# Kernel tuning notes

Measured on AMD Instinct MI355X. Metric: run time of the kernel, lower is better.

Reference implementation:

```python
import jax, jax.numpy as jnp
import numpy as np

B, S, D = 4, 4096, 64
D_MODEL = 64


def setup_inputs() -> dict:
    key = jax.random.key(0)
    kq, kk, kv, km = jax.random.split(key, 4)
    q = jax.random.normal(kq, (B, S, D), dtype=jnp.float32)
    k = jax.random.normal(kk, (B, S, D), dtype=jnp.float32)
    v = jax.random.normal(kv, (B, S, D), dtype=jnp.float32)
    mask = jax.random.uniform(km, (B, S, S), dtype=jnp.float32)
    return {"q": q, "k": k, "v": v, "mask": mask}


def reference(q, k, v, mask):
    dk = jnp.sqrt(jnp.asarray(D_MODEL, dtype=q.dtype))
    # [B,S,S] scores; multiplicative (non-additive) mask applied pre-softmax
    scaled_qk = jnp.einsum('bqd,bkd->bqk', q, k) / dk
    scaled_qk = scaled_qk * mask
    attn = jax.nn.softmax(scaled_qk, axis=-1)
    return jnp.einsum('bqk,bkd->bqd', attn, v)
```

## Files before the change

### kernel.cpp

```cpp
#include <hip/hip_runtime.h>
#include <hip/hip_bf16.h>

#define S_LEN 4096
#define DH 64
#define NBATCH 4

typedef __attribute__((ext_vector_type(8))) short bf16x8;
typedef __attribute__((ext_vector_type(4))) short bf16x4;
typedef __attribute__((ext_vector_type(4))) float f32x4;

static __device__ __forceinline__ short f2bf(float x) {
  __hip_bfloat16 h = __float2bfloat16(x);
  return *reinterpret_cast<short*>(&h);
}

#define MFMA(a, b, c) __builtin_amdgcn_mfma_f32_16x16x32_bf16((a), (b), (c), 0, 0, 0)

__global__ __launch_bounds__(256) void cvt_q_kernel(const float* __restrict__ q,
                                                    short* __restrict__ qb) {
  int i = (blockIdx.x * 256 + threadIdx.x) * 4;
  f32x4 x = *(const f32x4*)(q + i);
  bf16x4 o;
#pragma unroll
  for (int j = 0; j < 4; ++j) o[j] = f2bf(x[j]);
  *(bf16x4*)(qb + i) = o;
}

__global__ __launch_bounds__(256) void cvt_frag_kernel(const float* __restrict__ k,
                                                       const float* __restrict__ v,
                                                       short* __restrict__ kfrag,
                                                       short* __restrict__ vfrag) {
  __shared__ short kt[32][80];
  __shared__ short vt[32][80];
  const int t = threadIdx.x;
  const int b = blockIdx.x >> 7;
  const int i = blockIdx.x & 127;
  const size_t src0 = ((size_t)b * S_LEN + i * 32) * DH;
  {
    const int row = t >> 3, c0 = (t & 7) * 8;
    const f32x4 xk0 = *(const f32x4*)(k + src0 + row * DH + c0);
    const f32x4 xk1 = *(const f32x4*)(k + src0 + row * DH + c0 + 4);
    const f32x4 xv0 = *(const f32x4*)(v + src0 + row * DH + c0);
    const f32x4 xv1 = *(const f32x4*)(v + src0 + row * DH + c0 + 4);
#pragma unroll
    for (int j = 0; j < 4; ++j) {
      kt[row][c0 + j] = f2bf(xk0[j]);  kt[row][c0 + 4 + j] = f2bf(xk1[j]);
      vt[row][c0 + j] = f2bf(xv0[j]);  vt[row][c0 + 4 + j] = f2bf(xv1[j]);
    }
  }
  __syncthreads();
  const int c = t >> 6, l = t & 63;
  const size_t dst = (((size_t)(b * 128 + i) * 4 + c) * 64 + l) * 8;
  {
    const int kr = ((c >> 1) * 16) + (l & 15);
    const int d0 = ((c & 1) * 32) + (l >> 4) * 8;
    *(bf16x8*)(kfrag + dst) = *(const bf16x8*)&kt[kr][d0];
  }
  {
    bf16x8 f;
    const int col = c * 16 + (l & 15);
    const int r0 = (l >> 4) * 8;
#pragma unroll
    for (int j = 0; j < 8; ++j) f[j] = vt[r0 + j][col];
    *(bf16x8*)(vfrag + dst) = f;
  }
}

__global__ __launch_bounds__(512, 2) void fa_kernel(
    const short* __restrict__ qb, const short* __restrict__ kfrag,
    const short* __restrict__ vfrag, const float* __restrict__ mask,
    float* __restrict__ out) {
  __shared__ __align__(16) short kst[2][2][4][512];
  __shared__ __align__(16) short vst[2][2][4][512];
  __shared__ __align__(16) float mst[2][4096];
  __shared__ __align__(16) short lds_p[8][16][40];
  __shared__ float lds_O[8][16][64];
  __shared__ float lds_l[8][16];

  const int tid = threadIdx.x;
  const int w = tid >> 6;
  const int wq = w >> 1;
  const int wk = w & 1;
  const int lane = tid & 63;
  const int quad = lane >> 4;
  const int n16 = lane & 15;
  const int loff = lane * 8;

  const int vb = ((blockIdx.x & 7) << 5) | (blockIdx.x >> 3);
  const int b = vb >> 6;
  const int q0 = (vb & 63) << 6;

  const int qr = q0 + wq * 16 + n16;
  const short* qrow = qb + (size_t)(b * S_LEN + qr) * DH;
  const bf16x8 aQ0 = *(const bf16x8*)(qrow + quad * 8);
  const bf16x8 aQ1 = *(const bf16x8*)(qrow + 32 + quad * 8);

  f32x4 O0 = {0.f, 0.f, 0.f, 0.f}, O1 = O0, O2 = O0, O3 = O0;
  float lacc = 0.f;

  const int ksp = w >> 2, kfr = w & 3;
  const short* kbase =
      kfrag + (size_t)(b * 128 + ksp) * 2048 + kfr * 512 + loff;
  const short* vbase =
      vfrag + (size_t)(b * 128 + ksp) * 2048 + kfr * 512 + loff;
  const int srow0 = w * 8 + (lane >> 4);
  const int srow1 = srow0 + 4;
  const int sg = lane & 15;
  const float* msrc0 =
      mask + ((size_t)b * S_LEN + q0 + srow0) * S_LEN + sg * 4;
  const float* msrc1 =
      mask + ((size_t)b * S_LEN + q0 + srow1) * S_LEN + sg * 4;
  const int wslot0 = srow0 * 64 + (sg ^ (srow0 & 7)) * 4;
  const int wslot1 = srow1 * 64 + (sg ^ (srow1 & 7)) * 4;
  const int mr = wq * 16 + n16;
  const int rslot0 = mr * 64 + (((wk * 8 + quad) ^ (mr & 7)) * 4);
  const int rslot1 = mr * 64 + (((wk * 8 + 4 + quad) ^ (mr & 7)) * 4);

#define STEP(CUR, SS)                                                      \
  {                                                                        \
    const int sn_ = ((SS) + 1) & 63; \
    const bf16x8 kR = *(const bf16x8*)(kbase + (size_t)sn_ * 4096);        \
    const bf16x8 vR = *(const bf16x8*)(vbase + (size_t)sn_ * 4096);        \
    const f32x4 mR0 = *(const f32x4*)(msrc0 + sn_ * 64);                   \
    const f32x4 mR1 = *(const f32x4*)(msrc1 + sn_ * 64);                   \
    const f32x4 z = {0.f, 0.f, 0.f, 0.f};                                  \
    f32x4 s0 = MFMA(*(const bf16x8*)&kst[CUR][wk][0][loff], aQ0, z);       \
    s0 = MFMA(*(const bf16x8*)&kst[CUR][wk][1][loff], aQ1, s0);            \
    f32x4 s1 = MFMA(*(const bf16x8*)&kst[CUR][wk][2][loff], aQ0, z);       \
    s1 = MFMA(*(const bf16x8*)&kst[CUR][wk][3][loff], aQ1, s1);            \
    const f32x4 M0 = *(const f32x4*)&mst[CUR][rslot0];                     \
    const f32x4 M1 = *(const f32x4*)&mst[CUR][rslot1];                     \
    float p0_[4], p1_[4];                                                  \
    _Pragma("unroll") for (int r = 0; r < 4; ++r) {                        \
      p0_[r] = __expf(s0[r] * 0.125f * M0[r]);                             \
      p1_[r] = __expf(s1[r] * 0.125f * M1[r]);                             \
      lacc += p0_[r] + p1_[r];                                             \
    }                                                                      \
    bf16x4 w0_, w1_;                                                       \
    _Pragma("unroll") for (int r = 0; r < 4; ++r) {                        \
      w0_[r] = f2bf(p0_[r]); w1_[r] = f2bf(p1_[r]);                        \
    }                                                                      \
    *(bf16x4*)&lds_p[w][n16][quad * 4] = w0_;                              \
    *(bf16x4*)&lds_p[w][n16][16 + quad * 4] = w1_;                         \
    const bf16x8 aP = *(const bf16x8*)&lds_p[w][n16][quad * 8];            \
    O0 = MFMA(aP, *(const bf16x8*)&vst[CUR][wk][0][loff], O0);             \
    O1 = MFMA(aP, *(const bf16x8*)&vst[CUR][wk][1][loff], O1);             \
    O2 = MFMA(aP, *(const bf16x8*)&vst[CUR][wk][2][loff], O2);             \
    O3 = MFMA(aP, *(const bf16x8*)&vst[CUR][wk][3][loff], O3);             \
    *(bf16x8*)&kst[(CUR) ^ 1][ksp][kfr][loff] = kR;                        \
    *(bf16x8*)&vst[(CUR) ^ 1][ksp][kfr][loff] = vR;                        \
    *(f32x4*)&mst[(CUR) ^ 1][wslot0] = mR0;                                \
    *(f32x4*)&mst[(CUR) ^ 1][wslot1] = mR1;                                \
    __syncthreads();                                                       \
  }

  {
    const bf16x8 kR = *(const bf16x8*)(kbase);
    const bf16x8 vR = *(const bf16x8*)(vbase);
    const f32x4 mR0 = *(const f32x4*)(msrc0);
    const f32x4 mR1 = *(const f32x4*)(msrc1);
    *(bf16x8*)&kst[0][ksp][kfr][loff] = kR;
    *(bf16x8*)&vst[0][ksp][kfr][loff] = vR;
    *(f32x4*)&mst[0][wslot0] = mR0;
    *(f32x4*)&mst[0][wslot1] = mR1;
    __syncthreads();
  }

#pragma unroll 1
  for (int it = 0; it < 32; ++it) {
    STEP(0, 2 * it);
    STEP(1, 2 * it + 1);
  }
#undef STEP

  lacc += __shfl_xor(lacc, 16);
  lacc += __shfl_xor(lacc, 32);

#pragma unroll
  for (int r = 0; r < 4; ++r) {
    const int row = quad * 4 + r;
    lds_O[w][row][n16]      = O0[r];
    lds_O[w][row][16 + n16] = O1[r];
    lds_O[w][row][32 + n16] = O2[r];
    lds_O[w][row][48 + n16] = O3[r];
  }
  if (lane < 16) lds_l[w][lane] = lacc;
  __syncthreads();

  const int g = tid >> 7;
  const int r = (tid >> 3) & 15;
  const int c8 = (tid & 7) << 3;
  const int w0 = g * 2, w1 = g * 2 + 1;
  const float inv = 1.0f / (lds_l[w0][r] + lds_l[w1][r]);
  float* op = out + (size_t)(b * S_LEN + q0 + g * 16 + r) * DH + c8;
  f32x4 acc0, acc1;
#pragma unroll
  for (int j = 0; j < 4; ++j) {
    acc0[j] = (lds_O[w0][r][c8 + j]     + lds_O[w1][r][c8 + j])     * inv;
    acc1[j] = (lds_O[w0][r][c8 + 4 + j] + lds_O[w1][r][c8 + 4 + j]) * inv;
  }
  *(f32x4*)(op) = acc0;
  *(f32x4*)(op + 4) = acc1;
}

extern "C" void kernel_launch(void* const* d_in, const int* in_sizes, int n_in,
                              void* d_out, int out_size, void* d_ws, size_t ws_size,
                              hipStream_t stream) {
  const float* q = (const float*)d_in[0];
  const float* k = (const float*)d_in[1];
  const float* v = (const float*)d_in[2];
  const float* mask = (const float*)d_in[3];
  float* out = (float*)d_out;

  short* qb = (short*)d_ws;
  short* kfrag = qb + (size_t)NBATCH * S_LEN * DH;
  short* vfrag = kfrag + (size_t)NBATCH * S_LEN * DH;

  cvt_q_kernel<<<(NBATCH * S_LEN * DH) / 1024, 256, 0, stream>>>(q, qb);
  cvt_frag_kernel<<<NBATCH * 128, 256, 0, stream>>>(k, v, kfrag, vfrag);
  fa_kernel<<<NBATCH * 64, 512, 0, stream>>>(qb, kfrag, vfrag, mask, out);
}
```

Baseline: 393.4 us.

## Stage K/V/mask tiles via direct global-to-LDS loads with triple buffering

Replaces the register-staged double buffer with a three-deep LDS ring filled by global_load_lds, so K, V and mask tiles skip VGPRs and arrive two steps ahead. The XOR swizzle for the mask moves into the global source address, and a single waitcnt plus barrier per step replaces the per-step syncthreads. The epilogue buffers reuse the staging memory to keep LDS use in check. The cost is a larger LDS footprint, which may reduce blocks per CU, and a correctness risk from hand-written waitcnt accounting.

```diff
diff --git a/kernel.cpp b/kernel.cpp
--- a/kernel.cpp
+++ b/kernel.cpp
@@ -12,6 +12,12 @@
 static __device__ __forceinline__ short f2bf(float x) {
   __hip_bfloat16 h = __float2bfloat16(x);
   return *reinterpret_cast<short*>(&h);
+}
+
+static __device__ __forceinline__ void gl_lds16(const void* g, void* l) {
+  __builtin_amdgcn_global_load_lds(
+      (const __attribute__((address_space(1))) void*)g,
+      (__attribute__((address_space(3))) void*)l, 16, 0, 0);
 }
 
 #define MFMA(a, b, c) __builtin_amdgcn_mfma_f32_16x16x32_bf16((a), (b), (c), 0, 0, 0)
@@ -70,12 +76,8 @@
     const short* __restrict__ qb, const short* __restrict__ kfrag,
     const short* __restrict__ vfrag, const float* __restrict__ mask,
     float* __restrict__ out) {
-  __shared__ __align__(16) short kst[2][2][4][512];
-  __shared__ __align__(16) short vst[2][2][4][512];
-  __shared__ __align__(16) float mst[2][4096];
+  __shared__ __align__(16) char sstage[3 * 32768];
   __shared__ __align__(16) short lds_p[8][16][40];
-  __shared__ float lds_O[8][16][64];
-  __shared__ float lds_l[8][16];
 
   const int tid = threadIdx.x;
   const int w = tid >> 6;
@@ -107,29 +109,42 @@
   const int srow1 = srow0 + 4;
   const int sg = lane & 15;
   const float* msrc0 =
-      mask + ((size_t)b * S_LEN + q0 + srow0) * S_LEN + sg * 4;
+      mask + ((size_t)b * S_LEN + q0 + srow0) * S_LEN + (sg ^ (srow0 & 7)) * 4;
   const float* msrc1 =
-      mask + ((size_t)b * S_LEN + q0 + srow1) * S_LEN + sg * 4;
-  const int wslot0 = srow0 * 64 + (sg ^ (srow0 & 7)) * 4;
-  const int wslot1 = srow1 * 64 + (sg ^ (srow1 & 7)) * 4;
+      mask + ((size_t)b * S_LEN + q0 + srow1) * S_LEN + (sg ^ (srow1 & 7)) * 4;
+
+  const int kdst = ksp * 4096 + kfr * 1024;
+  const int vdst = 8192 + kdst;
+  const int mdst0 = 16384 + w * 2048;
+  const int mdst1 = mdst0 + 1024;
+
   const int mr = wq * 16 + n16;
-  const int rslot0 = mr * 64 + (((wk * 8 + quad) ^ (mr & 7)) * 4);
-  const int rslot1 = mr * 64 + (((wk * 8 + 4 + quad) ^ (mr & 7)) * 4);
-
-#define STEP(CUR, SS)                                                      \
+  const int rslot0 = mr * 64 + ((wk * 8 + quad) ^ (mr & 7)) * 4;
+  const int rslot1 = mr * 64 + ((wk * 8 + 4 + quad) ^ (mr & 7)) * 4;
+
+  asm volatile("s_waitcnt vmcnt(0)" ::: "memory");
+
+#define STAGE(SB, SS)                                        \
+  {                                                          \
+    const int sn_ = (SS) & 63;                               \
+    gl_lds16(kbase + (size_t)sn_ * 4096, (SB) + kdst);       \
+    gl_lds16(vbase + (size_t)sn_ * 4096, (SB) + vdst);       \
+    gl_lds16(msrc0 + (size_t)sn_ * 64, (SB) + mdst0);        \
+    gl_lds16(msrc1 + (size_t)sn_ * 64, (SB) + mdst1);        \
+  }
+
+#define COMPUTE(SB)                                                        \
   {                                                                        \
-    const int sn_ = ((SS) + 1) & 63; \
-    const bf16x8 kR = *(const bf16x8*)(kbase + (size_t)sn_ * 4096);        \
-    const bf16x8 vR = *(const bf16x8*)(vbase + (size_t)sn_ * 4096);        \
-    const f32x4 mR0 = *(const f32x4*)(msrc0 + sn_ * 64);                   \
-    const f32x4 mR1 = *(const f32x4*)(msrc1 + sn_ * 64);                   \
+    const short* kk_ = (const short*)((SB) + wk * 4096) + loff;            \
+    const short* vv_ = (const short*)((SB) + 8192 + wk * 4096) + loff;     \
+    const float* mm_ = (const float*)((SB) + 16384);                       \
     const f32x4 z = {0.f, 0.f, 0.f, 0.f};                                  \
-    f32x4 s0 = MFMA(*(const bf16x8*)&kst[CUR][wk][0][loff], aQ0, z);       \
-    s0 = MFMA(*(const bf16x8*)&kst[CUR][wk][1][loff], aQ1, s0);            \
-    f32x4 s1 = MFMA(*(const bf16x8*)&kst[CUR][wk][2][loff], aQ0, z);       \
-    s1 = MFMA(*(const bf16x8*)&kst[CUR][wk][3][loff], aQ1, s1);            \
-    const f32x4 M0 = *(const f32x4*)&mst[CUR][rslot0];                     \
-    const f32x4 M1 = *(const f32x4*)&mst[CUR][rslot1];                     \
+    f32x4 s0 = MFMA(*(const bf16x8*)(kk_), aQ0, z);                        \
+    s0 = MFMA(*(const bf16x8*)(kk_ + 512), aQ1, s0);                       \
+    f32x4 s1 = MFMA(*(const bf16x8*)(kk_ + 1024), aQ0, z);                 \
+    s1 = MFMA(*(const bf16x8*)(kk_ + 1536), aQ1, s1);                      \
+    const f32x4 M0 = *(const f32x4*)(mm_ + rslot0);                        \
+    const f32x4 M1 = *(const f32x4*)(mm_ + rslot1);                        \
     float p0_[4], p1_[4];                                                  \
     _Pragma("unroll") for (int r = 0; r < 4; ++r) {                        \
       p0_[r] = __expf(s0[r] * 0.125f * M0[r]);                             \
@@ -143,35 +158,32 @@
     *(bf16x4*)&lds_p[w][n16][quad * 4] = w0_;                              \
     *(bf16x4*)&lds_p[w][n16][16 + quad * 4] = w1_;                         \
     const bf16x8 aP = *(const bf16x8*)&lds_p[w][n16][quad * 8];            \
-    O0 = MFMA(aP, *(const bf16x8*)&vst[CUR][wk][0][loff], O0);             \
-    O1 = MFMA(aP, *(const bf16x8*)&vst[CUR][wk][1][loff], O1);             \
-    O2 = MFMA(aP, *(const bf16x8*)&vst[CUR][wk][2][loff], O2);             \
-    O3 = MFMA(aP, *(const bf16x8*)&vst[CUR][wk][3][loff], O3);             \
-    *(bf16x8*)&kst[(CUR) ^ 1][ksp][kfr][loff] = kR;                        \
-    *(bf16x8*)&vst[(CUR) ^ 1][ksp][kfr][loff] = vR;                        \
-    *(f32x4*)&mst[(CUR) ^ 1][wslot0] = mR0;                                \
-    *(f32x4*)&mst[(CUR) ^ 1][wslot1] = mR1;                                \
-    __syncthreads();                                                       \
-  }
-
-  {
-    const bf16x8 kR = *(const bf16x8*)(kbase);
-    const bf16x8 vR = *(const bf16x8*)(vbase);
-    const f32x4 mR0 = *(const f32x4*)(msrc0);
-    const f32x4 mR1 = *(const f32x4*)(msrc1);
-    *(bf16x8*)&kst[0][ksp][kfr][loff] = kR;
-    *(bf16x8*)&vst[0][ksp][kfr][loff] = vR;
-    *(f32x4*)&mst[0][wslot0] = mR0;
-    *(f32x4*)&mst[0][wslot1] = mR1;
-    __syncthreads();
-  }
+    O0 = MFMA(aP, *(const bf16x8*)(vv_), O0);                              \
+    O1 = MFMA(aP, *(const bf16x8*)(vv_ + 512), O1);                        \
+    O2 = MFMA(aP, *(const bf16x8*)(vv_ + 1024), O2);                       \
+    O3 = MFMA(aP, *(const bf16x8*)(vv_ + 1536), O3);                       \
+  }
+
+  char* bufA = sstage;
+  char* bufB = sstage + 32768;
+  char* bufC = sstage + 65536;
+  STAGE(bufA, 0);
+  STAGE(bufB, 1);
 
 #pragma unroll 1
-  for (int it = 0; it < 32; ++it) {
-    STEP(0, 2 * it);
-    STEP(1, 2 * it + 1);
-  }
-#undef STEP
+  for (int s = 0; s < 64; ++s) {
+    asm volatile("s_waitcnt vmcnt(4)\n\ts_barrier" ::: "memory");
+    STAGE(bufC, s + 2);
+    COMPUTE(bufA);
+    char* t_ = bufA; bufA = bufB; bufB = bufC; bufC = t_;
+  }
+#undef STAGE
+#undef COMPUTE
+
+  asm volatile("s_waitcnt vmcnt(0)\n\ts_barrier" ::: "memory");
+
+  float* ldsO = (float*)sstage;
+  float* ldsl = (float*)(sstage + 32768);
 
   lacc += __shfl_xor(lacc, 16);
   lacc += __shfl_xor(lacc, 32);
@@ -179,25 +191,28 @@
 #pragma unroll
   for (int r = 0; r < 4; ++r) {
     const int row = quad * 4 + r;
-    lds_O[w][row][n16]      = O0[r];
-    lds_O[w][row][16 + n16] = O1[r];
-    lds_O[w][row][32 + n16] = O2[r];
-    lds_O[w][row][48 + n16] = O3[r];
-  }
-  if (lane < 16) lds_l[w][lane] = lacc;
+    float* od = ldsO + (w * 16 + row) * 64;
+    od[n16]      = O0[r];
+    od[16 + n16] = O1[r];
+    od[32 + n16] = O2[r];
+    od[48 + n16] = O3[r];
+  }
+  if (lane < 16) ldsl[w * 16 + lane] = lacc;
   __syncthreads();
 
   const int g = tid >> 7;
-  const int r = (tid >> 3) & 15;
+  const int rr = (tid >> 3) & 15;
   const int c8 = (tid & 7) << 3;
-  const int w0 = g * 2, w1 = g * 2 + 1;
-  const float inv = 1.0f / (lds_l[w0][r] + lds_l[w1][r]);
-  float* op = out + (size_t)(b * S_LEN + q0 + g * 16 + r) * DH + c8;
+  const int wa = g * 2, wb = g * 2 + 1;
+  const float inv = 1.0f / (ldsl[wa * 16 + rr] + ldsl[wb * 16 + rr]);
+  const float* oap = ldsO + (wa * 16 + rr) * 64 + c8;
+  const float* obp = ldsO + (wb * 16 + rr) * 64 + c8;
+  float* op = out + (size_t)(b * S_LEN + q0 + g * 16 + rr) * DH + c8;
   f32x4 acc0, acc1;
 #pragma unroll
   for (int j = 0; j < 4; ++j) {
-    acc0[j] = (lds_O[w0][r][c8 + j]     + lds_O[w1][r][c8 + j])     * inv;
-    acc1[j] = (lds_O[w0][r][c8 + 4 + j] + lds_O[w1][r][c8 + 4 + j]) * inv;
+    acc0[j] = (oap[j]     + obp[j])     * inv;
+    acc1[j] = (oap[4 + j] + obp[4 + j]) * inv;
   }
   *(f32x4*)(op) = acc0;
   *(f32x4*)(op + 4) = acc1;
```

Measured after the change: 390.1 us. About the same (-0.9%).
